# Kernel optimization log

Measured on AMD Instinct MI355X. Metric: run time of the kernel, lower is better.

The kernel has to match this reference:

```python
import jax, jax.numpy as jnp
import numpy as np

B, N, T, D, M, HOPS = 32, 300, 12, 64, 16, 2

def setup_inputs() -> dict:
    key = jax.random.key(0)
    ks = jax.random.split(key, 12)
    inp = {
        "X": jax.random.normal(ks[0], (B, D, N, T), dtype=jnp.float32),
        "timeEmbedding": jax.random.normal(ks[1], (B, N, T, D), dtype=jnp.float32),
        "adjW": jax.random.normal(ks[2], (N, D), dtype=jnp.float32) * (1.0 / np.sqrt(D)),
        "adjB": jnp.zeros((N,), dtype=jnp.float32),
        "trainW1": jax.random.normal(ks[3], (N, M), dtype=jnp.float32) * 0.1,
        "trainW2": jax.random.normal(ks[4], (M, D * D), dtype=jnp.float32) * 0.1,
        "alpha1": jax.random.normal(ks[5], (N, M), dtype=jnp.float32) * 0.1,
        "alpha2": jax.random.normal(ks[6], (M, N), dtype=jnp.float32) * 0.1,
        "beta1": jax.random.normal(ks[7], (N, M), dtype=jnp.float32) * 0.1,
        "beta2": jax.random.normal(ks[8], (M, N), dtype=jnp.float32) * 0.1,
        "gcnW": jax.random.normal(ks[9], (D, D * (HOPS + 1)), dtype=jnp.float32) * (1.0 / np.sqrt(D * (HOPS + 1))),
        "gcnB": jnp.zeros((D,), dtype=jnp.float32),
    }
    return inp

def reference(X, timeEmbedding, adjW, adjB, trainW1, trainW2, alpha1, alpha2, beta1, beta2, gcnW, gcnB):
    # timeEmbedding: [B,N,T,D] -> [B,T,N,D]
    te = jnp.transpose(timeEmbedding, (0, 2, 1, 3))
    # learned adjacency: A[b,t,n,k]
    A = jnp.sin(jnp.einsum('btnd,kd->btnk', te, adjW) + adjB)  # Linear(dmodel->N)
    A = (alpha1 @ alpha2) * A            # elementwise scale by [N,N], broadcast over b,t
    A = jax.nn.relu(A + beta1 @ beta2)
    # X: [B,D,N,T] -> [B,T,N,D]
    Xp = jnp.transpose(X, (0, 3, 2, 1))
    # per-node weight matrices [N,D,D]
    W = (trainW1 @ trainW2).reshape(N, D, D)
    Hs = [Xp]
    Hb = Xp
    for _ in range(HOPS):
        Hnow = jnp.einsum('btnk,btkd->btnd', A, Hb)      # adjacency aggregation
        Hnow = jnp.einsum('btnk,nkd->btnd', Hnow, W)     # per-node distinct matmul
        pre = Xp + Hnow
        Hnow = jax.nn.sigmoid(pre) * jnp.tanh(pre)        # gated residual
        Hs.append(Hnow)
        Hb = Hnow
    H = jnp.concatenate(Hs, axis=3)                       # [B,T,N,D*(hops+1)]
    Hout = jnp.einsum('btnf,df->btnd', H, gcnW) + gcnB    # gcnLinear (dropout = identity in eval)
    return jnp.transpose(Hout, (0, 3, 2, 1))              # [B,D,N,T]
```

## Files before the change

kernel.cpp:

```cpp
#include <hip/hip_runtime.h>

#define Nq 300
#define Tq 12
#define Dq 64
#define Mq 16
#define BTq 384
#define DDq (Dq*Dq)
#define Fq (Dq*3)
#define NP 320

typedef short bf8_t __attribute__((ext_vector_type(8)));
typedef float f4_t  __attribute__((ext_vector_type(4)));

__device__ __forceinline__ unsigned short f2bf(float f) {
    unsigned u = __float_as_uint(f);
    u = (u + 0x7FFFu + ((u >> 16) & 1u)) >> 16;
    return (unsigned short)u;
}
__device__ __forceinline__ float bf2f(unsigned short u) {
    return __uint_as_float((unsigned)u << 16);
}
__device__ __forceinline__ float4 ld4(const float* p) { return *(const float4*)p; }

__device__ __forceinline__ bf8_t pack8(float4 a, float4 b) {
    bf8_t r;
    r[0] = (short)f2bf(a.x); r[1] = (short)f2bf(a.y);
    r[2] = (short)f2bf(a.z); r[3] = (short)f2bf(a.w);
    r[4] = (short)f2bf(b.x); r[5] = (short)f2bf(b.y);
    r[6] = (short)f2bf(b.z); r[7] = (short)f2bf(b.w);
    return r;
}

__device__ __forceinline__ float gatef(float p) {
    float pc = fminf(fmaxf(p, -30.f), 30.f);
    float sig = 1.f / (1.f + __expf(-pc));
    float e2  = __expf(2.f * pc);
    float th  = (e2 - 1.f) / (e2 + 1.f);
    return sig * th;
}

__global__ void __launch_bounds__(256) kprep_all(
    const float* __restrict__ a1, const float* __restrict__ a2,
    const float* __restrict__ b1, const float* __restrict__ b2,
    const float* __restrict__ w1, const float* __restrict__ w2,
    const float* __restrict__ adjW, const float* __restrict__ adjB,
    const float* __restrict__ X,
    unsigned* __restrict__ ABt, unsigned short* __restrict__ Wt,
    unsigned short* __restrict__ adjWb, float* __restrict__ adjBp,
    unsigned short* __restrict__ Xp_t, unsigned short* __restrict__ Xp_nb)
{
    __shared__ char smem[64 * 308 * 2];
    const int vb = blockIdx.x;
    const int tid = threadIdx.x;

    if (vb < 400) {
        const int tile = vb;
        const int reg = tid & 3, lane = tid >> 2;
        const int nt = tile % 5;  int r1 = tile / 5;
        const int w  = r1 % 4;    int r2 = r1 / 4;
        const int c  = r2 % 5;    const int qi = r2 / 5;
        const int n = qi*80 + nt*16 + (lane & 15);
        const int k = c*64 + w*16 + (lane >> 4)*4 + reg;
        unsigned outv = 0u;
        if (n < Nq && k < Nq) {
            float sa = 0.f, sb = 0.f;
            #pragma unroll
            for (int m = 0; m < Mq; ++m) {
                sa = fmaf(a1[n*Mq+m], a2[m*Nq+k], sa);
                sb = fmaf(b1[n*Mq+m], b2[m*Nq+k], sb);
            }
            outv = ((unsigned)f2bf(sb) << 16) | (unsigned)f2bf(sa);
        }
        ABt[tile*256 + tid] = outv;
    } else if (vb < 700) {
        float* sT = (float*)smem;
        __shared__ float sw1[Mq];
        const int n = vb - 400;
        if (tid < Mq) sw1[tid] = w1[n*Mq + tid];
        __syncthreads();
        for (int i = tid; i < DDq; i += 256) {
            int k = i >> 6, d = i & 63;
            float s = 0.f;
            #pragma unroll
            for (int m = 0; m < Mq; ++m) s = fmaf(sw1[m], w2[m*DDq + i], s);
            sT[d*65 + k] = s;
        }
        __syncthreads();
        for (int i = tid; i < DDq; i += 256) {
            int d = i >> 6, k = i & 63;
            Wt[(size_t)n*DDq + i] = f2bf(sT[d*65 + k]);
        }
    } else if (vb < 780) {
        int e = (vb - 700) * 256 + tid;
        if (e < NP * 64) {
            int k = e >> 6, d = e & 63;
            adjWb[e] = (k < Nq) ? f2bf(adjW[k*Dq + d]) : (unsigned short)0;
        }
        if (e < NP) adjBp[e] = (e < Nq) ? adjB[e] : 0.f;
    } else {
        unsigned short* sT = (unsigned short*)smem;
        const int bx = vb - 780;
        const int b = bx / 12, tile = bx % 12;
        const int n0 = tile * 25;
        for (int i = tid; i < 64 * 300; i += 256) {
            int d = i / 300, j = i - d * 300;
            sT[d*308 + j] = f2bf(X[(size_t)(b*64 + d)*3600 + n0*12 + j]);
        }
        __syncthreads();
        for (int wi = tid; wi < 12 * 64 * 25; wi += 256) {
            int nl = wi % 25, rem = wi / 25;
            int d = rem % 64, t = rem / 64;
            Xp_t[((size_t)(b*Tq + t)*64 + d)*NP + n0 + nl] = sT[d*308 + nl*12 + t];
        }
        if (tile == 11) {
            for (int wi = tid; wi < 12 * 64 * 20; wi += 256) {
                int e = wi % 20, rem = wi / 20;
                int d = rem % 64, t = rem / 64;
                Xp_t[((size_t)(b*Tq + t)*64 + d)*NP + 300 + e] = 0;
            }
        }
        for (int wi = tid; wi < 25 * 12 * 64; wi += 256) {
            int d = wi & 63, rem = wi >> 6;
            int t = rem % 12, nl = rem / 12;
            Xp_nb[((size_t)(n0 + nl)*BTq + b*Tq + t)*64 + d] = sT[d*308 + nl*12 + t];
        }
    }
}

__global__ void __launch_bounds__(256) ktr2(const unsigned short* __restrict__ Hnb,
                                            unsigned short* __restrict__ Ht) {
    __shared__ unsigned short sT[64 * 308];
    const int bt = blockIdx.x;
    const int tid = threadIdx.x;
    for (int i = tid; i < 300 * 64; i += 256) {
        int n = i >> 6, d = i & 63;
        sT[d*308 + n] = Hnb[((size_t)n*BTq + bt)*64 + d];
    }
    __syncthreads();
    for (int wi = tid; wi < 64 * 80; wi += 256) {
        int kq = wi % 80, d = wi / 80;
        ushort4 o;
        int k = kq * 4;
        o.x = (k+0 < Nq) ? sT[d*308 + k+0] : (unsigned short)0;
        o.y = (k+1 < Nq) ? sT[d*308 + k+1] : (unsigned short)0;
        o.z = (k+2 < Nq) ? sT[d*308 + k+2] : (unsigned short)0;
        o.w = (k+3 < Nq) ? sT[d*308 + k+3] : (unsigned short)0;
        *(ushort4*)&Ht[((size_t)bt*64 + d)*NP + k] = o;
    }
}

__global__ void __launch_bounds__(256) kfuse(
    const float* __restrict__ te,
    const unsigned short* __restrict__ adjWb,
    const float* __restrict__ adjBp,
    const unsigned* __restrict__ ABt,
    const unsigned short* __restrict__ Hb_t,
    unsigned short* __restrict__ Hout_nb)
{
    __shared__ unsigned short sPl[2][80 * 72];
    const int bt = blockIdx.x >> 2, qi = blockIdx.x & 3;
    const int b = bt / Tq, t = bt - b * Tq;
    const int nbase = qi * 80;
    const int tid = threadIdx.x;
    const int w = tid >> 6, lane = tid & 63, quad = lane >> 4, l16 = lane & 15;
    const int dcol = w*16 + l16;

    bf8_t tb0[5], tb1[5];
    #pragma unroll
    for (int nt = 0; nt < 5; ++nt) {
        int n = nbase + nt*16 + l16; if (n > Nq-1) n = Nq-1;
        const float* ter = te + (((size_t)b*Nq + n)*Tq + t)*Dq;
        tb0[nt] = pack8(ld4(ter + quad*8),      ld4(ter + quad*8 + 4));
        tb1[nt] = pack8(ld4(ter + 32 + quad*8), ld4(ter + 36 + quad*8));
    }
    f4_t accO[5];
    #pragma unroll
    for (int rt = 0; rt < 5; ++rt) accO[rt] = (f4_t){0.f, 0.f, 0.f, 0.f};

    for (int c = 0; c < 5; ++c) {
        const int cbase = c * 64;
        const unsigned short* ar = adjWb + (cbase + w*16 + l16)*64;
        bf8_t ka0 = *(const bf8_t*)(ar + quad*8);
        bf8_t ka1 = *(const bf8_t*)(ar + 32 + quad*8);
        float4 bias4 = ld4(adjBp + cbase + w*16 + quad*4);
        const unsigned* abbase = ABt + ((((size_t)qi*5 + c)*4 + w)*5)*256 + lane*4;
        unsigned short* sp = sPl[c & 1];
        #pragma unroll
        for (int nt = 0; nt < 5; ++nt) {
            f4_t p = {0.f, 0.f, 0.f, 0.f};
            p = __builtin_amdgcn_mfma_f32_16x16x32_bf16(ka0, tb0[nt], p, 0, 0, 0);
            p = __builtin_amdgcn_mfma_f32_16x16x32_bf16(ka1, tb1[nt], p, 0, 0, 0);
            uint4 ab = *(const uint4*)(abbase + nt*256);
            ushort4 o4;
            {
                float sv = __sinf(p[0] + bias4.x);
                o4.x = f2bf(fmaxf(fmaf(__uint_as_float(ab.x << 16), sv,
                                       __uint_as_float(ab.x & 0xFFFF0000u)), 0.f));
            }
            {
                float sv = __sinf(p[1] + bias4.y);
                o4.y = f2bf(fmaxf(fmaf(__uint_as_float(ab.y << 16), sv,
                                       __uint_as_float(ab.y & 0xFFFF0000u)), 0.f));
            }
            {
                float sv = __sinf(p[2] + bias4.z);
                o4.z = f2bf(fmaxf(fmaf(__uint_as_float(ab.z << 16), sv,
                                       __uint_as_float(ab.z & 0xFFFF0000u)), 0.f));
            }
            {
                float sv = __sinf(p[3] + bias4.w);
                o4.w = f2bf(fmaxf(fmaf(__uint_as_float(ab.w << 16), sv,
                                       __uint_as_float(ab.w & 0xFFFF0000u)), 0.f));
            }
            *(ushort4*)&sp[(nt*16 + l16)*72 + w*16 + quad*4] = o4;
        }
        __syncthreads();
        const unsigned short* hr = Hb_t + ((size_t)bt*64 + dcol)*NP + cbase;
        bf8_t v0 = *(const bf8_t*)(hr + quad*8);
        bf8_t v1 = *(const bf8_t*)(hr + 32 + quad*8);
        #pragma unroll
        for (int rt = 0; rt < 5; ++rt) {
            bf8_t p0 = *(const bf8_t*)&sp[(rt*16 + l16)*72 + quad*8];
            bf8_t p1 = *(const bf8_t*)&sp[(rt*16 + l16)*72 + 32 + quad*8];
            accO[rt] = __builtin_amdgcn_mfma_f32_16x16x32_bf16(p0, v0, accO[rt], 0, 0, 0);
            accO[rt] = __builtin_amdgcn_mfma_f32_16x16x32_bf16(p1, v1, accO[rt], 0, 0, 0);
        }
    }
    #pragma unroll
    for (int rt = 0; rt < 5; ++rt) {
        #pragma unroll
        for (int reg = 0; reg < 4; ++reg) {
            int ng = nbase + rt*16 + quad*4 + reg;
            if (ng < Nq)
                Hout_nb[((size_t)ng*BTq + bt)*64 + dcol] = f2bf(accO[rt][reg]);
        }
    }
}

__global__ void __launch_bounds__(256) kmm(
    const unsigned short* __restrict__ Hagg_nb,
    const unsigned short* __restrict__ Xp_nb,
    const unsigned short* __restrict__ Wt,
    unsigned short* __restrict__ Hout_nb)
{
    const int n = blockIdx.x >> 2, qi = blockIdx.x & 3;
    const int bt0 = qi * 96;
    const int tid = threadIdx.x;
    const int w = tid >> 6, lane = tid & 63, quad = lane >> 4, l16 = lane & 15;
    const int dcol = w*16 + l16;
    const unsigned short* wn = Wt + (size_t)n * DDq + dcol*64;
    bf8_t v0 = *(const bf8_t*)(wn + quad*8);
    bf8_t v1 = *(const bf8_t*)(wn + 32 + quad*8);
    f4_t acc[6];
    #pragma unroll
    for (int rt = 0; rt < 6; ++rt) acc[rt] = (f4_t){0.f, 0.f, 0.f, 0.f};
    #pragma unroll
    for (int rt = 0; rt < 6; ++rt) {
        int r = bt0 + rt*16 + l16;
        const unsigned short* row = Hagg_nb + ((size_t)n*BTq + r)*64;
        bf8_t a0 = *(const bf8_t*)(row + quad*8);
        bf8_t a1 = *(const bf8_t*)(row + 32 + quad*8);
        acc[rt] = __builtin_amdgcn_mfma_f32_16x16x32_bf16(a0, v0, acc[rt], 0, 0, 0);
        acc[rt] = __builtin_amdgcn_mfma_f32_16x16x32_bf16(a1, v1, acc[rt], 0, 0, 0);
    }
    __syncthreads();
    #pragma unroll
    for (int rt = 0; rt < 6; ++rt) {
        #pragma unroll
        for (int reg = 0; reg < 4; ++reg) {
            int r = bt0 + rt*16 + quad*4 + reg;
            size_t idx = ((size_t)n*BTq + r)*64 + dcol;
            float xp = bf2f(Xp_nb[idx]);
            Hout_nb[idx] = f2bf(gatef(xp + acc[rt][reg]));
        }
    }
}

__global__ void __launch_bounds__(256) kgcn(
    const unsigned short* __restrict__ Xp_nb, const unsigned short* __restrict__ H1_nb,
    const unsigned short* __restrict__ H2_nb, const float* __restrict__ gcnW,
    const float* __restrict__ gcnB, float* __restrict__ out)
{
    const int b = blockIdx.x / 19, tile = blockIdx.x % 19;
    const int n0 = tile * 16;
    const int rows = (tile == 18) ? 144 : 192;
    const int tid = threadIdx.x;
    const int w = tid >> 6, lane = tid & 63, quad = lane >> 4, l16 = lane & 15;
    const int dcol = w*16 + l16;
    const float bias = gcnB[dcol];
    f4_t acc[12];
    #pragma unroll
    for (int rt = 0; rt < 12; ++rt) acc[rt] = (f4_t){0.f, 0.f, 0.f, 0.f};
    const unsigned short* bufs[3] = {Xp_nb, H1_nb, H2_nb};
    #pragma unroll
    for (int c = 0; c < 3; ++c) {
        const unsigned short* buf = bufs[c];
        const float* gwr = gcnW + (size_t)dcol*Fq + c*Dq;
        bf8_t v0 = pack8(ld4(gwr + quad*8),      ld4(gwr + quad*8 + 4));
        bf8_t v1 = pack8(ld4(gwr + 32 + quad*8), ld4(gwr + 36 + quad*8));
        #pragma unroll
        for (int rt = 0; rt < 12; ++rt) {
            int r = rt*16 + l16;
            int nl = r / 12, t = r - nl*12;
            int n = n0 + nl; if (n > Nq-1) n = Nq-1;
            const unsigned short* row = buf + ((size_t)n*BTq + b*Tq + t)*64;
            bf8_t a0 = *(const bf8_t*)(row + quad*8);
            bf8_t a1 = *(const bf8_t*)(row + 32 + quad*8);
            acc[rt] = __builtin_amdgcn_mfma_f32_16x16x32_bf16(a0, v0, acc[rt], 0, 0, 0);
            acc[rt] = __builtin_amdgcn_mfma_f32_16x16x32_bf16(a1, v1, acc[rt], 0, 0, 0);
        }
    }
    float* outd = out + (size_t)(b*Dq + dcol)*3600 + n0*12;
    #pragma unroll
    for (int rt = 0; rt < 12; ++rt) {
        if (rt*16 < rows) {
            int r0 = rt*16 + quad*4;
            float4 o = make_float4(acc[rt][0] + bias, acc[rt][1] + bias,
                                   acc[rt][2] + bias, acc[rt][3] + bias);
            *(float4*)&outd[r0] = o;
        }
    }
}

extern "C" void kernel_launch(void* const* d_in, const int* in_sizes, int n_in,
                              void* d_out, int out_size, void* d_ws, size_t ws_size,
                              hipStream_t stream) {
    (void)in_sizes; (void)n_in; (void)out_size; (void)ws_size;
    const float* X    = (const float*)d_in[0];
    const float* te   = (const float*)d_in[1];
    const float* adjW = (const float*)d_in[2];
    const float* adjB = (const float*)d_in[3];
    const float* w1   = (const float*)d_in[4];
    const float* w2   = (const float*)d_in[5];
    const float* a1   = (const float*)d_in[6];
    const float* a2   = (const float*)d_in[7];
    const float* b1   = (const float*)d_in[8];
    const float* b2   = (const float*)d_in[9];
    const float* gW   = (const float*)d_in[10];
    const float* gB   = (const float*)d_in[11];
    float* out = (float*)d_out;

    char* ws = (char*)d_ws;
    unsigned*       ABt    = (unsigned*)      (ws);
    unsigned short* adjWb  = (unsigned short*)(ws + 409600);
    float*          adjBp  = (float*)         (ws + 450560);
    unsigned short* Wt     = (unsigned short*)(ws + 451840);
    unsigned short* Xp_t   = (unsigned short*)(ws + 2909440);
    unsigned short* Xp_nb  = (unsigned short*)(ws + 18638080);
    unsigned short* Hagg   = (unsigned short*)(ws + 33383680);
    unsigned short* H1_nb  = (unsigned short*)(ws + 48129280);
    unsigned short* H1_t   = (unsigned short*)(ws + 62874880);

    hipLaunchKernelGGL(kprep_all, dim3(1164), dim3(256), 0, stream,
                       a1, a2, b1, b2, w1, w2, adjW, adjB, X,
                       ABt, Wt, adjWb, adjBp, Xp_t, Xp_nb);
    hipLaunchKernelGGL(kfuse, dim3(1536), dim3(256), 0, stream, te, adjWb, adjBp, ABt, Xp_t, Hagg);
    hipLaunchKernelGGL(kmm,   dim3(1200), dim3(256), 0, stream, Hagg, Xp_nb, Wt, H1_nb);
    hipLaunchKernelGGL(ktr2,  dim3(384),  dim3(256), 0, stream, H1_nb, H1_t);
    hipLaunchKernelGGL(kfuse, dim3(1536), dim3(256), 0, stream, te, adjWb, adjBp, ABt, H1_t, Hagg);
    hipLaunchKernelGGL(kmm,   dim3(1200), dim3(256), 0, stream, Hagg, Xp_nb, Wt, Hagg);
    hipLaunchKernelGGL(kgcn,  dim3(608), dim3(256), 0, stream, Xp_nb, H1_nb, Hagg, gW, gB, out);
}
```

Before: 322.9 us.

## Materialize adjacency once and reuse it across both hops

Adds a kernel kA that computes the learned adjacency (sin of the projection, scaled and shifted, then relu) once per (b,t) and stores it as padded bf16 in the workspace. A separate aggregation kernel, kagg, reads it back for each hop, so the sin and projection work is no longer recomputed inside the fused kernel on every hop. kagg also remaps block indices so blocks sharing a (b,t) land on the same XCD. The cost is writing a buffer of about 74 MB and reading it twice. The new path runs only when the workspace is large enough; otherwise the old fused path is kept, now also writing the hop-1 transpose into Xp_t.

```diff
diff --git a/kernel.cpp b/kernel.cpp
--- a/kernel.cpp
+++ b/kernel.cpp
@@ -149,6 +149,119 @@
     }
 }
 
+__global__ void __launch_bounds__(256) kA(
+    const float* __restrict__ te,
+    const unsigned short* __restrict__ adjWb,
+    const float* __restrict__ adjBp,
+    const unsigned* __restrict__ ABt,
+    unsigned short* __restrict__ At)
+{
+    const int bt = blockIdx.x >> 2, qi = blockIdx.x & 3;
+    const int b = bt / Tq, t = bt - b * Tq;
+    const int nbase = qi * 80;
+    const int tid = threadIdx.x;
+    const int w = tid >> 6, lane = tid & 63, quad = lane >> 4, l16 = lane & 15;
+
+    bf8_t tb0[5], tb1[5];
+    #pragma unroll
+    for (int nt = 0; nt < 5; ++nt) {
+        int n = nbase + nt*16 + l16; if (n > Nq-1) n = Nq-1;
+        const float* ter = te + (((size_t)b*Nq + n)*Tq + t)*Dq;
+        tb0[nt] = pack8(ld4(ter + quad*8),      ld4(ter + quad*8 + 4));
+        tb1[nt] = pack8(ld4(ter + 32 + quad*8), ld4(ter + 36 + quad*8));
+    }
+    #pragma unroll
+    for (int c = 0; c < 5; ++c) {
+        const int cbase = c * 64;
+        const unsigned short* ar = adjWb + (cbase + w*16 + l16)*64;
+        bf8_t ka0 = *(const bf8_t*)(ar + quad*8);
+        bf8_t ka1 = *(const bf8_t*)(ar + 32 + quad*8);
+        float4 bias4 = ld4(adjBp + cbase + w*16 + quad*4);
+        const unsigned* abbase = ABt + ((((size_t)qi*5 + c)*4 + w)*5)*256 + lane*4;
+        #pragma unroll
+        for (int nt = 0; nt < 5; ++nt) {
+            f4_t p = {0.f, 0.f, 0.f, 0.f};
+            p = __builtin_amdgcn_mfma_f32_16x16x32_bf16(ka0, tb0[nt], p, 0, 0, 0);
+            p = __builtin_amdgcn_mfma_f32_16x16x32_bf16(ka1, tb1[nt], p, 0, 0, 0);
+            uint4 ab = *(const uint4*)(abbase + nt*256);
+            ushort4 o4;
+            {
+                float sv = __sinf(p[0] + bias4.x);
+                o4.x = f2bf(fmaxf(fmaf(__uint_as_float(ab.x << 16), sv,
+                                       __uint_as_float(ab.x & 0xFFFF0000u)), 0.f));
+            }
+            {
+                float sv = __sinf(p[1] + bias4.y);
+                o4.y = f2bf(fmaxf(fmaf(__uint_as_float(ab.y << 16), sv,
+                                       __uint_as_float(ab.y & 0xFFFF0000u)), 0.f));
+            }
+            {
+                float sv = __sinf(p[2] + bias4.z);
+                o4.z = f2bf(fmaxf(fmaf(__uint_as_float(ab.z << 16), sv,
+                                       __uint_as_float(ab.z & 0xFFFF0000u)), 0.f));
+            }
+            {
+                float sv = __sinf(p[3] + bias4.w);
+                o4.w = f2bf(fmaxf(fmaf(__uint_as_float(ab.w << 16), sv,
+                                       __uint_as_float(ab.w & 0xFFFF0000u)), 0.f));
+            }
+            int n = nbase + nt*16 + l16;
+            if (n < Nq)
+                *(ushort4*)&At[((size_t)bt*Nq + n)*NP + cbase + w*16 + quad*4] = o4;
+        }
+    }
+}
+
+__global__ void __launch_bounds__(256) kagg(
+    const unsigned short* __restrict__ At,
+    const unsigned short* __restrict__ Hb_t,
+    unsigned short* __restrict__ Hout_nb)
+{
+    const int g = blockIdx.x;
+    const int xcd = g & 7, li = g >> 3;
+    const int bt = xcd * 48 + (li % 48), qi = li / 48;
+    const int tid = threadIdx.x;
+    const int w = tid >> 6, lane = tid & 63, quad = lane >> 4, l16 = lane & 15;
+    const int dcol = w*16 + l16;
+    const int nbase = qi * 80;
+
+    const unsigned short* hrow = Hb_t + ((size_t)bt*64 + dcol)*NP;
+    const unsigned short* ab0  = At + (size_t)bt*Nq*NP;
+    size_t aoff[5];
+    #pragma unroll
+    for (int rt = 0; rt < 5; ++rt) {
+        int r = nbase + rt*16 + l16; if (r > Nq-1) r = Nq-1;
+        aoff[rt] = (size_t)r * NP;
+    }
+    f4_t accO[5];
+    #pragma unroll
+    for (int rt = 0; rt < 5; ++rt) accO[rt] = (f4_t){0.f, 0.f, 0.f, 0.f};
+
+    #pragma unroll
+    for (int c = 0; c < 5; ++c) {
+        const int cbase = c * 64;
+        bf8_t v0 = *(const bf8_t*)(hrow + cbase + quad*8);
+        bf8_t v1 = *(const bf8_t*)(hrow + cbase + 32 + quad*8);
+        #pragma unroll
+        for (int rt = 0; rt < 5; ++rt) {
+            const unsigned short* arr = ab0 + aoff[rt] + cbase;
+            bf8_t p0 = *(const bf8_t*)(arr + quad*8);
+            bf8_t p1 = *(const bf8_t*)(arr + 32 + quad*8);
+            accO[rt] = __builtin_amdgcn_mfma_f32_16x16x32_bf16(p0, v0, accO[rt], 0, 0, 0);
+            accO[rt] = __builtin_amdgcn_mfma_f32_16x16x32_bf16(p1, v1, accO[rt], 0, 0, 0);
+        }
+    }
+    #pragma unroll
+    for (int rt = 0; rt < 5; ++rt) {
+        #pragma unroll
+        for (int reg = 0; reg < 4; ++reg) {
+            int ng = nbase + rt*16 + quad*4 + reg;
+            if (ng < Nq)
+                Hout_nb[((size_t)ng*BTq + bt)*64 + dcol] = f2bf(accO[rt][reg]);
+        }
+    }
+}
+
 __global__ void __launch_bounds__(256) kfuse(
     const float* __restrict__ te,
     const unsigned short* __restrict__ adjWb,
@@ -325,7 +438,7 @@
 extern "C" void kernel_launch(void* const* d_in, const int* in_sizes, int n_in,
                               void* d_out, int out_size, void* d_ws, size_t ws_size,
                               hipStream_t stream) {
-    (void)in_sizes; (void)n_in; (void)out_size; (void)ws_size;
+    (void)in_sizes; (void)n_in; (void)out_size;
     const float* X    = (const float*)d_in[0];
     const float* te   = (const float*)d_in[1];
     const float* adjW = (const float*)d_in[2];
@@ -349,15 +462,28 @@
     unsigned short* Xp_nb  = (unsigned short*)(ws + 18638080);
     unsigned short* Hagg   = (unsigned short*)(ws + 33383680);
     unsigned short* H1_nb  = (unsigned short*)(ws + 48129280);
-    unsigned short* H1_t   = (unsigned short*)(ws + 62874880);
+    unsigned short* At     = (unsigned short*)(ws + 62874880);
+    const size_t NEED_NEW = 136602880;
 
     hipLaunchKernelGGL(kprep_all, dim3(1164), dim3(256), 0, stream,
                        a1, a2, b1, b2, w1, w2, adjW, adjB, X,
                        ABt, Wt, adjWb, adjBp, Xp_t, Xp_nb);
-    hipLaunchKernelGGL(kfuse, dim3(1536), dim3(256), 0, stream, te, adjWb, adjBp, ABt, Xp_t, Hagg);
-    hipLaunchKernelGGL(kmm,   dim3(1200), dim3(256), 0, stream, Hagg, Xp_nb, Wt, H1_nb);
-    hipLaunchKernelGGL(ktr2,  dim3(384),  dim3(256), 0, stream, H1_nb, H1_t);
-    hipLaunchKernelGGL(kfuse, dim3(1536), dim3(256), 0, stream, te, adjWb, adjBp, ABt, H1_t, Hagg);
-    hipLaunchKernelGGL(kmm,   dim3(1200), dim3(256), 0, stream, Hagg, Xp_nb, Wt, Hagg);
+
+    if (ws_size >= NEED_NEW) {
+        hipLaunchKernelGGL(kA, dim3(1536), dim3(256), 0, stream, te, adjWb, adjBp, ABt, At);
+        hipLaunchKernelGGL(kagg, dim3(1536), dim3(256), 0, stream, At, Xp_t, Hagg);
+        hipLaunchKernelGGL(kmm,  dim3(1200), dim3(256), 0, stream, Hagg, Xp_nb, Wt, H1_nb);
+        hipLaunchKernelGGL(ktr2, dim3(384),  dim3(256), 0, stream, H1_nb, Xp_t);
+        hipLaunchKernelGGL(kagg, dim3(1536), dim3(256), 0, stream, At, Xp_t, Hagg);
+        hipLaunchKernelGGL(kmm,  dim3(1200), dim3(256), 0, stream, Hagg, Xp_nb, Wt, Hagg);
+    } else {
+        unsigned short* H1_t = (unsigned short*)(ws + 62874880 + 14745600);
+        H1_t = (unsigned short*)(ws + 62874880);
+        hipLaunchKernelGGL(kfuse, dim3(1536), dim3(256), 0, stream, te, adjWb, adjBp, ABt, Xp_t, Hagg);
+        hipLaunchKernelGGL(kmm,   dim3(1200), dim3(256), 0, stream, Hagg, Xp_nb, Wt, H1_nb);
+        hipLaunchKernelGGL(ktr2,  dim3(384),  dim3(256), 0, stream, H1_nb, Xp_t);
+        hipLaunchKernelGGL(kfuse, dim3(1536), dim3(256), 0, stream, te, adjWb, adjBp, ABt, Xp_t, Hagg);
+        hipLaunchKernelGGL(kmm,   dim3(1200), dim3(256), 0, stream, Hagg, Xp_nb, Wt, Hagg);
+    }
     hipLaunchKernelGGL(kgcn,  dim3(608), dim3(256), 0, stream, Xp_nb, H1_nb, Hagg, gW, gB, out);
 }
```

New measurement: 366.5 us. 1.14x slower.
